# Kernel optimization log

Measured on AMD Instinct MI355X. Metric: run time of the kernel, lower is better.

## Reference

```python
import jax, jax.numpy as jnp
import numpy as np

S, B, E, H, V, L = 128, 64, 512, 1024, 10000, 2


def setup_inputs() -> dict:
    key = jax.random.key(0)
    ks = jax.random.split(key, 10)
    s = 0.02  # weight scale ~ uniform(-k,k) magnitude
    return {
        "inputs": jax.random.randint(ks[0], (S, B), 0, V),
        "hidden": jnp.zeros((L, B, H), jnp.float32),
        "emb": jax.random.normal(ks[1], (V, E), jnp.float32) * 0.1,
        "Wx0": jax.random.normal(ks[2], (3, H, E), jnp.float32) * s,
        "Uh0": jax.random.normal(ks[3], (3, H, H), jnp.float32) * s,
        "b0": jax.random.normal(ks[4], (3, H), jnp.float32) * s,
        "Wx1": jax.random.normal(ks[5], (3, H, H), jnp.float32) * s,
        "Uh1": jax.random.normal(ks[6], (3, H, H), jnp.float32) * s,
        "b1": jax.random.normal(ks[7], (3, H), jnp.float32) * s,
        "Wd": jax.random.normal(ks[8], (V, H), jnp.float32) * 0.1,
        "bd": jnp.zeros((V,), jnp.float32),
    }


def _gru_cell(xp, h, U, b):
    # xp: (3,B,H) precomputed input projections in [r,z,h] order
    r = jax.nn.sigmoid(xp[0] + h @ U[0].T + b[0])
    z = jax.nn.sigmoid(xp[1] + h @ U[1].T + b[1])
    h_tilde = jnp.tanh(xp[2] + (r * h) @ U[2].T + b[2])
    return (1.0 - z) * h + z * h_tilde


def reference(inputs, hidden, emb, Wx0, Uh0, b0, Wx1, Uh1, b1, Wd, bd):
    x_embs = emb[inputs]                                   # [S,B,E]
    # precompute layer-0 input projections across all timesteps
    xa0 = jnp.einsum("sbe,goe->sgbo", x_embs, Wx0)        # [S,3,B,H]

    def step(carry, xa0_t):
        h0, h1 = carry
        h0n = _gru_cell(xa0_t, h0, Uh0, b0)
        xp1 = jnp.einsum("bk,gok->gbo", h0n, Wx1)          # [3,B,H]
        h1n = _gru_cell(xp1, h1, Uh1, b1)
        return (h0n, h1n), h1n

    (h0f, h1f), hs1 = jax.lax.scan(step, (hidden[0], hidden[1]), xa0)
    logits = jnp.einsum("sbh,vh->sbv", hs1, Wd) + bd       # [S,B,V]
    return logits, jnp.stack([h0f, h1f])
```

## Files before the change

### kernel.cpp

```cpp
#include <hip/hip_runtime.h>
#include <hip/hip_bf16.h>

#define SLEN 128
#define BAT 64
#define EDIM 512
#define HDIM 1024
#define VOC 10000
#define VPAD 10112
#define NWG_REC 192
#define TPB_REC 512

typedef short v8s __attribute__((ext_vector_type(8)));
typedef float v4f __attribute__((ext_vector_type(4)));
typedef unsigned short u16;

__device__ __forceinline__ u16 f2bf(float f) {
  unsigned u = __float_as_uint(f);
  u += 0x7fffu + ((u >> 16) & 1u);
  return (u16)(u >> 16);
}
__device__ __forceinline__ float bf2f(u16 b) {
  return __uint_as_float(((unsigned)b) << 16);
}
__device__ __forceinline__ float sigm(float x) { return 1.f / (1.f + __expf(-x)); }
__device__ __forceinline__ float tanh_f(float x) { return 1.f - 2.f / (1.f + __expf(2.f * x)); }

__device__ __forceinline__ void st_f32(float* p, float v) {
  __hip_atomic_store(p, v, __ATOMIC_RELAXED, __HIP_MEMORY_SCOPE_AGENT);
}
__device__ __forceinline__ float ld_f32(const float* p) {
  return __hip_atomic_load(p, __ATOMIC_RELAXED, __HIP_MEMORY_SCOPE_AGENT);
}
__device__ __forceinline__ float ld_bf16(const unsigned* base, int elem) {
  unsigned pr = __hip_atomic_load(base + (elem >> 1), __ATOMIC_RELAXED, __HIP_MEMORY_SCOPE_AGENT);
  return bf2f((u16)((elem & 1) ? (pr >> 16) : (pr & 0xffffu)));
}
__device__ __forceinline__ void st_bf16_pair(unsigned* base, int elem, u16 val, int l) {
  unsigned p = (unsigned)__shfl_xor((int)val, 1);
  if ((l & 1) == 0)
    __hip_atomic_store(base + (elem >> 1), (unsigned)val | (p << 16),
                       __ATOMIC_RELAXED, __HIP_MEMORY_SCOPE_AGENT);
}

__device__ __forceinline__ void gbar(int* bar, int ph, int wg, int t) {
  asm volatile("s_waitcnt vmcnt(0) lgkmcnt(0)" ::: "memory");
  __syncthreads();
  if (t == 0)
    __hip_atomic_store(&bar[wg], ph, __ATOMIC_RELAXED, __HIP_MEMORY_SCOPE_AGENT);
  if (wg == 0) {
    if (t < 64) {
      for (;;) {
        int v0 = __hip_atomic_load(&bar[t],       __ATOMIC_RELAXED, __HIP_MEMORY_SCOPE_AGENT);
        int v1 = __hip_atomic_load(&bar[64 + t],  __ATOMIC_RELAXED, __HIP_MEMORY_SCOPE_AGENT);
        int v2 = __hip_atomic_load(&bar[128 + t], __ATOMIC_RELAXED, __HIP_MEMORY_SCOPE_AGENT);
        if (__all((v0 >= ph) & (v1 >= ph) & (v2 >= ph))) break;
        __builtin_amdgcn_s_sleep(1);
      }
      if (t == 0)
        __hip_atomic_store(&bar[256], ph, __ATOMIC_RELAXED, __HIP_MEMORY_SCOPE_AGENT);
    }
  } else if (t < 64) {
    while (__hip_atomic_load(&bar[256], __ATOMIC_RELAXED, __HIP_MEMORY_SCOPE_AGENT) < ph)
      __builtin_amdgcn_s_sleep(4);
  }
  __syncthreads();
}

__device__ __forceinline__ v4f gemm_sc(const char* apl, const char* bcl, int swz, int lk2) {
  v8s a[8];
  v4f acc0{0.f, 0.f, 0.f, 0.f}, acc1{0.f, 0.f, 0.f, 0.f};
#pragma unroll
  for (int j = 0; j < 8; ++j)
    asm volatile("global_load_dwordx4 %0, %1, off offset:%2 sc0 sc1"
                 : "=v"(a[j]) : "v"(apl), "i"(j * 64));
#pragma unroll
  for (int ks = 0; ks < 32; ++ks) {
    asm volatile("s_waitcnt vmcnt(%0)" :: "i"((ks < 24) ? 7 : (31 - ks)));
    __builtin_amdgcn_sched_barrier(0x3F6);
    v8s b = *(const v8s*)(bcl + ((ks * 64 + lk2) ^ swz));
    if (ks & 1) acc1 = __builtin_amdgcn_mfma_f32_16x16x32_bf16(a[ks & 7], b, acc1, 0, 0, 0);
    else        acc0 = __builtin_amdgcn_mfma_f32_16x16x32_bf16(a[ks & 7], b, acc0, 0, 0, 0);
    if (ks < 24)
      asm volatile("global_load_dwordx4 %0, %1, off offset:%2 sc0 sc1"
                   : "=v"(a[ks & 7]) : "v"(apl), "i"((ks + 8) * 64));
  }
  return acc0 + acc1;
}

__global__ void __launch_bounds__(512, 2) k_recur(
    const u16* __restrict__ Uh0b, const u16* __restrict__ Wx1b, const u16* __restrict__ Uh1b,
    const float* __restrict__ b0, const float* __restrict__ b1,
    const u16* __restrict__ xa0,
    float* __restrict__ h0f, u16* __restrict__ h0b,
    float* __restrict__ h1f, u16* __restrict__ h1b,
    u16* __restrict__ a2, float* __restrict__ z0,
    u16* __restrict__ a5, float* __restrict__ z1,
    u16* __restrict__ xp1,
    u16* __restrict__ hs1,
    float* __restrict__ outh,
    int* __restrict__ bar) {
  extern __shared__ char smem[];
  const int wg = blockIdx.x;
  const int t = threadIdx.x;
  const int w = t >> 6;
  const int l = t & 63;
  const int lr = l & 15;
  const int lk2 = (l >> 4) * 16;
  const int rg = w >> 1, cg = w & 1;
  const int rbase1 = rg * 16 + ((l >> 4) << 2);
  const int rbase2 = w * 16 + ((l >> 4) << 2);

  unsigned* a2u  = (unsigned*)a2;
  unsigned* a5u  = (unsigned*)a5;
  unsigned* h0bu = (unsigned*)h0b;
  unsigned* h1bu = (unsigned*)h1b;
  unsigned* xpu  = (unsigned*)xp1;

  {
    const u16* w1src; int w1row0;
    if (wg < 64)       { w1src = Uh0b; w1row0 = wg * 32; }
    else if (wg < 160) { w1src = Wx1b; w1row0 = (wg - 64) * 32; }
    else               { w1src = Uh1b; w1row0 = 2048 + (wg - 160) * 32; }
    const u16* w2src; int w2row0;
    if (wg < 64) { w2src = Uh0b; w2row0 = 2048 + wg * 16; }
    else         { w2src = Uh1b; w2row0 = (wg - 64) * 16; }
    for (int i = t; i < 4096; i += TPB_REC) {
      int c = i >> 7, j = i & 127;
      v8s v = *(const v8s*)(w1src + (size_t)(w1row0 + c) * HDIM + j * 8);
      int off = c * 2048 + ((j * 16) ^ ((c & 7) << 4));
      *(v8s*)(smem + off) = v;
    }
    for (int i = t; i < 2048; i += TPB_REC) {
      int c = i >> 7, j = i & 127;
      v8s v = *(const v8s*)(w2src + (size_t)(w2row0 + c) * HDIM + j * 8);
      int off = 65536 + c * 2048 + ((j * 16) ^ ((c & 7) << 4));
      *(v8s*)(smem + off) = v;
    }
    __syncthreads();
  }

  const char* bb1 = smem + (cg * 16 + lr) * 2048;
  const int swz1 = ((cg * 16 + lr) & 7) << 4;
  const char* bb2 = smem + 65536 + lr * 2048;
  const int swz2 = (lr & 7) << 4;

  for (int T = 0; T <= SLEN + 1; ++T) {
    if (wg < 64) {
      if (T < SLEN) {
        const int cglob = wg * 32 + cg * 16 + lr;
        const int g = cglob >> 10;
        const int o = cglob & 1023;
        const float bias = b0[g * HDIM + o];
        float xv[4], hv[4];
#pragma unroll
        for (int r = 0; r < 4; ++r) {
          int b = rbase1 + r;
          xv[r] = bf2f(xa0[((T * 3 + g) * BAT + b) * HDIM + o]);
          if (g == 0) hv[r] = ld_f32(&h0f[b * HDIM + o]);
        }
        const char* apl = (const char*)h0b + (rg * 16 + lr) * 2048 + lk2;
        v4f acc = gemm_sc(apl, bb1, swz1, lk2);
#pragma unroll
        for (int r = 0; r < 4; ++r) {
          int b = rbase1 + r;
          float s = sigm(acc[r] + xv[r] + bias);
          if (g == 0) st_bf16_pair(a2u, b * HDIM + o, f2bf(s * hv[r]), l);
          else        st_f32(&z0[b * HDIM + o], s);
        }
      }
    } else if (wg < 160) {
      if (T >= 1 && T <= SLEN) {
        const int n = (wg - 64) * 32 + cg * 16 + lr;
        const char* apl = (const char*)h0b + (rg * 16 + lr) * 2048 + lk2;
        v4f acc = gemm_sc(apl, bb1, swz1, lk2);
        unsigned* xp = xpu + (((T - 1) & 1) * (BAT * 3 * HDIM) >> 1);
#pragma unroll
        for (int r = 0; r < 4; ++r)
          st_bf16_pair(xp, (rbase1 + r) * 3072 + n, f2bf(acc[r]), l);
      }
    } else {
      if (T >= 2) {
        const int t5 = T - 2;
        const int o = (wg - 160) * 32 + cg * 16 + lr;
        const unsigned* xp = xpu + (((t5 & 1) * (BAT * 3 * HDIM)) >> 1);
        const float bias = b1[2 * HDIM + o];
        float xv[4], zv[4], hv[4];
#pragma unroll
        for (int r = 0; r < 4; ++r) {
          int b = rbase1 + r;
          xv[r] = ld_bf16(xp, b * 3072 + 2048 + o);
          zv[r] = ld_f32(&z1[b * HDIM + o]);
          hv[r] = ld_f32(&h1f[b * HDIM + o]);
        }
        const char* apl = (const char*)a5 + (rg * 16 + lr) * 2048 + lk2;
        v4f acc = gemm_sc(apl, bb1, swz1, lk2);
#pragma unroll
        for (int r = 0; r < 4; ++r) {
          int b = rbase1 + r;
          float ht = tanh_f(xv[r] + acc[r] + bias);
          float hn = (1.f - zv[r]) * hv[r] + zv[r] * ht;
          u16 hb = f2bf(hn);
          st_f32(&h1f[b * HDIM + o], hn);
          st_bf16_pair(h1bu, b * HDIM + o, hb, l);
          hs1[((size_t)t5 * BAT + b) * HDIM + o] = hb;
          if (t5 == SLEN - 1) outh[(size_t)BAT * HDIM + b * HDIM + o] = hn;
        }
      }
    }
    gbar(bar, 2 * T + 1, wg, t);
    if (w < 4) {
      if (wg < 64) {
        if (T < SLEN) {
          const int o = wg * 16 + lr;
          const float bias = b0[2 * HDIM + o];
          float xv[4], zv[4], hv[4];
#pragma unroll
          for (int r = 0; r < 4; ++r) {
            int b = rbase2 + r;
            xv[r] = bf2f(xa0[((T * 3 + 2) * BAT + b) * HDIM + o]);
            zv[r] = ld_f32(&z0[b * HDIM + o]);
            hv[r] = ld_f32(&h0f[b * HDIM + o]);
          }
          const char* apl = (const char*)a2 + (w * 16 + lr) * 2048 + lk2;
          v4f acc = gemm_sc(apl, bb2, swz2, lk2);
#pragma unroll
          for (int r = 0; r < 4; ++r) {
            int b = rbase2 + r;
            float ht = tanh_f(xv[r] + acc[r] + bias);
            float hn = (1.f - zv[r]) * hv[r] + zv[r] * ht;
            st_f32(&h0f[b * HDIM + o], hn);
            st_bf16_pair(h0bu, b * HDIM + o, f2bf(hn), l);
            if (T == SLEN - 1) outh[b * HDIM + o] = hn;
          }
        }
      } else {
        if (T >= 1 && T <= SLEN) {
          const int t4 = T - 1;
          const int cglob = (wg - 64) * 16 + lr;
          const int g = cglob >> 10;
          const int o = cglob & 1023;
          const unsigned* xp = xpu + (((t4 & 1) * (BAT * 3 * HDIM)) >> 1);
          const float bias = b1[g * HDIM + o];
          float xv[4], hv[4];
#pragma unroll
          for (int r = 0; r < 4; ++r) {
            int b = rbase2 + r;
            xv[r] = ld_bf16(xp, b * 3072 + g * HDIM + o);
            if (g == 0) hv[r] = ld_f32(&h1f[b * HDIM + o]);
          }
          const char* apl = (const char*)h1b + (w * 16 + lr) * 2048 + lk2;
          v4f acc = gemm_sc(apl, bb2, swz2, lk2);
#pragma unroll
          for (int r = 0; r < 4; ++r) {
            int b = rbase2 + r;
            float s = sigm(acc[r] + xv[r] + bias);
            if (g == 0) st_bf16_pair(a5u, b * HDIM + o, f2bf(s * hv[r]), l);
            else        st_f32(&z1[b * HDIM + o], s);
          }
        }
      }
    }
    gbar(bar, 2 * T + 2, wg, t);
  }
}

template <int MODE>
__global__ void __launch_bounds__(256) k_gemm(
    const u16* __restrict__ A, const u16* __restrict__ Bw,
    const int* __restrict__ gidx, const float* __restrict__ bias,
    void* __restrict__ Out) {
  constexpr int K = MODE ? 1024 : 512;
  constexpr int NB_N = MODE ? (VPAD / 128) : (3072 / 128);

  __shared__ u16 sA[128 * 64];
  __shared__ u16 sB[128 * 64];

  const int nwg = gridDim.x;
  const int cpx = nwg >> 3;
  const int bid = blockIdx.x;
  const int swz = (bid & 7) * cpx + (bid >> 3);
  const int bm = swz / NB_N, bn = swz % NB_N;
  const int m0 = bm * 128, n0 = bn * 128;

  const int t = threadIdx.x;
  const int w = t >> 6, l = t & 63;
  const int lr = l & 15, lk = (l >> 4) * 8;
  const int wm = (w >> 1) * 64, wn = (w & 1) * 64;
  const int kc = (t & 7) * 8;

  int arowg[4];
#pragma unroll
  for (int i = 0; i < 4; ++i) {
    int row = m0 + i * 32 + (t >> 3);
    arowg[i] = (MODE == 0) ? gidx[row] : row;
  }
  int brow[4];
#pragma unroll
  for (int i = 0; i < 4; ++i) brow[i] = n0 + i * 32 + (t >> 3);

  v4f acc[4][4];
#pragma unroll
  for (int mi = 0; mi < 4; ++mi)
#pragma unroll
    for (int ni = 0; ni < 4; ++ni) acc[mi][ni] = v4f{0.f, 0.f, 0.f, 0.f};

  for (int k0 = 0; k0 < K; k0 += 64) {
    __syncthreads();
#pragma unroll
    for (int i = 0; i < 4; ++i) {
      const u16* src = A + (size_t)arowg[i] * K + k0 + kc;
      __builtin_amdgcn_global_load_lds((const __attribute__((address_space(1))) void*)src,
                                       (__attribute__((address_space(3))) void*)(sA + i * 2048 + w * 512),
                                       16, 0, 0);
    }
#pragma unroll
    for (int i = 0; i < 4; ++i) {
      const u16* src = Bw + (size_t)brow[i] * K + k0 + kc;
      __builtin_amdgcn_global_load_lds((const __attribute__((address_space(1))) void*)src,
                                       (__attribute__((address_space(3))) void*)(sB + i * 2048 + w * 512),
                                       16, 0, 0);
    }
    asm volatile("s_waitcnt vmcnt(0)" ::: "memory");
    __syncthreads();
#pragma unroll
    for (int ks = 0; ks < 2; ++ks) {
      v8s af[4], bfr[4];
#pragma unroll
      for (int mi = 0; mi < 4; ++mi) af[mi] = *(const v8s*)&sA[(wm + mi * 16 + lr) * 64 + ks * 32 + lk];
#pragma unroll
      for (int ni = 0; ni < 4; ++ni) bfr[ni] = *(const v8s*)&sB[(wn + ni * 16 + lr) * 64 + ks * 32 + lk];
#pragma unroll
      for (int mi = 0; mi < 4; ++mi)
#pragma unroll
        for (int ni = 0; ni < 4; ++ni)
          acc[mi][ni] = __builtin_amdgcn_mfma_f32_16x16x32_bf16(af[mi], bfr[ni], acc[mi][ni], 0, 0, 0);
    }
  }

#pragma unroll
  for (int mi = 0; mi < 4; ++mi)
#pragma unroll
    for (int ni = 0; ni < 4; ++ni)
#pragma unroll
      for (int r = 0; r < 4; ++r) {
        int grow = m0 + wm + mi * 16 + ((l >> 4) << 2) + r;
        int gcol = n0 + wn + ni * 16 + lr;
        float v = acc[mi][ni][r];
        if (MODE == 0) {
          int s = grow >> 6, b = grow & 63;
          int g = gcol >> 10, o = gcol & 1023;
          ((u16*)Out)[(((size_t)s * 3 + g) * BAT + b) * HDIM + o] = f2bf(v);
        } else {
          if (gcol < VOC) ((float*)Out)[(size_t)grow * VOC + gcol] = v + bias[gcol];
        }
      }
}

__global__ void k_cvt(const float* __restrict__ src, u16* __restrict__ dst, int n, int nsrc) {
  int i = (blockIdx.x * 256 + threadIdx.x) * 4;
  if (i >= n) return;
#pragma unroll
  for (int j = 0; j < 4; ++j) {
    int idx = i + j;
    if (idx < n) dst[idx] = (idx < nsrc) ? f2bf(src[idx]) : (u16)0;
  }
}

__global__ void k_init(const float* __restrict__ hidden,
                       float* h0f, u16* h0b, float* h1f, u16* h1b, int* bar) {
  int i = blockIdx.x * 256 + threadIdx.x;
  if (i < BAT * HDIM) {
    float v0 = hidden[i];
    float v1 = hidden[BAT * HDIM + i];
    h0f[i] = v0; h0b[i] = f2bf(v0);
    h1f[i] = v1; h1b[i] = f2bf(v1);
  }
  if (i < 512) bar[i] = 0;
}

extern "C" void kernel_launch(void* const* d_in, const int* in_sizes, int n_in,
                              void* d_out, int out_size, void* d_ws, size_t ws_size,
                              hipStream_t stream) {
  const int*   inp = (const int*)d_in[0];
  const float* hid = (const float*)d_in[1];
  const float* emb = (const float*)d_in[2];
  const float* Wx0 = (const float*)d_in[3];
  const float* Uh0 = (const float*)d_in[4];
  const float* b0  = (const float*)d_in[5];
  const float* Wx1 = (const float*)d_in[6];
  const float* Uh1 = (const float*)d_in[7];
  const float* b1  = (const float*)d_in[8];
  const float* Wd  = (const float*)d_in[9];
  const float* bd  = (const float*)d_in[10];

  char* ws = (char*)d_ws;
  size_t off = 0;
  auto alloc = [&](size_t bytes) {
    void* p = ws + off;
    off = (off + bytes + 255) & ~(size_t)255;
    return p;
  };
  u16* emb_b = (u16*)alloc(sizeof(u16) * (size_t)VOC * EDIM);
  u16* Wx0_b = (u16*)alloc(sizeof(u16) * 3 * HDIM * EDIM);
  u16* Uh0_b = (u16*)alloc(sizeof(u16) * 3 * HDIM * HDIM);
  u16* Wx1_b = (u16*)alloc(sizeof(u16) * 3 * HDIM * HDIM);
  u16* Uh1_b = (u16*)alloc(sizeof(u16) * 3 * HDIM * HDIM);
  u16* Wd_b  = (u16*)alloc(sizeof(u16) * (size_t)VPAD * HDIM);
  u16* xa0_b = (u16*)alloc(sizeof(u16) * (size_t)SLEN * 3 * BAT * HDIM);
  u16* hs1_b = (u16*)alloc(sizeof(u16) * (size_t)SLEN * BAT * HDIM);
  u16* xp1   = (u16*)alloc(sizeof(u16) * 2 * BAT * 3 * HDIM);
  float* h0f = (float*)alloc(sizeof(float) * BAT * HDIM);
  float* h1f = (float*)alloc(sizeof(float) * BAT * HDIM);
  u16* h0b   = (u16*)alloc(sizeof(u16) * BAT * HDIM);
  u16* h1b   = (u16*)alloc(sizeof(u16) * BAT * HDIM);
  u16* a2    = (u16*)alloc(sizeof(u16) * BAT * HDIM);
  u16* a5    = (u16*)alloc(sizeof(u16) * BAT * HDIM);
  float* z0  = (float*)alloc(sizeof(float) * BAT * HDIM);
  float* z1  = (float*)alloc(sizeof(float) * BAT * HDIM);
  int* bar   = (int*)alloc(sizeof(int) * 512);

  float* logits = (float*)d_out;
  float* outh = logits + (size_t)SLEN * BAT * VOC;

  auto cvt = [&](const float* s, u16* d, int n, int nsrc) {
    k_cvt<<<dim3((n / 4 + 255) / 256), dim3(256), 0, stream>>>(s, d, n, nsrc);
  };
  cvt(emb, emb_b, VOC * EDIM, VOC * EDIM);
  cvt(Wx0, Wx0_b, 3 * HDIM * EDIM, 3 * HDIM * EDIM);
  cvt(Uh0, Uh0_b, 3 * HDIM * HDIM, 3 * HDIM * HDIM);
  cvt(Wx1, Wx1_b, 3 * HDIM * HDIM, 3 * HDIM * HDIM);
  cvt(Uh1, Uh1_b, 3 * HDIM * HDIM, 3 * HDIM * HDIM);
  cvt(Wd, Wd_b, VPAD * HDIM, VOC * HDIM);
  k_init<<<dim3(256), dim3(256), 0, stream>>>(hid, h0f, h0b, h1f, h1b, bar);

  k_gemm<0><<<dim3(64 * 24), dim3(256), 0, stream>>>(emb_b, Wx0_b, inp, (const float*)nullptr, (void*)xa0_b);

  (void)hipFuncSetAttribute(reinterpret_cast<const void*>(k_recur),
                            hipFuncAttributeMaxDynamicSharedMemorySize, 96 * 1024);
  k_recur<<<dim3(NWG_REC), dim3(TPB_REC), 96 * 1024, stream>>>(
      Uh0_b, Wx1_b, Uh1_b, b0, b1, xa0_b,
      h0f, h0b, h1f, h1b, a2, z0, a5, z1, xp1, hs1_b, outh, bar);

  k_gemm<1><<<dim3(64 * 79), dim3(256), 0, stream>>>(hs1_b, Wd_b, (const int*)nullptr, bd, d_out);
}
```

Before: 3.015 ms.

## Stage activation tiles through LDS and rebalance second-phase GEMM across fewer workgroups

Replaces per-wave direct global loads of the activation operand with a cooperative, double-buffered LDS staging pipeline, so each 64x1024 activation tile is fetched once per workgroup instead of once per wave row-group. The second barrier phase now uses 96 workgroups each computing 32 columns with all 8 waves, instead of 192 workgroups using only 4 waves. The grid barrier becomes decentralized, with every workgroup polling all flags rather than waiting on a master's release flag. LDS grows to 144KB, which limits occupancy to one workgroup per CU and adds per-chunk __syncthreads inside the GEMM.

```diff
diff --git a/kernel.cpp b/kernel.cpp
--- a/kernel.cpp
+++ b/kernel.cpp
@@ -47,47 +47,58 @@
   __syncthreads();
   if (t == 0)
     __hip_atomic_store(&bar[wg], ph, __ATOMIC_RELAXED, __HIP_MEMORY_SCOPE_AGENT);
-  if (wg == 0) {
-    if (t < 64) {
-      for (;;) {
-        int v0 = __hip_atomic_load(&bar[t],       __ATOMIC_RELAXED, __HIP_MEMORY_SCOPE_AGENT);
-        int v1 = __hip_atomic_load(&bar[64 + t],  __ATOMIC_RELAXED, __HIP_MEMORY_SCOPE_AGENT);
-        int v2 = __hip_atomic_load(&bar[128 + t], __ATOMIC_RELAXED, __HIP_MEMORY_SCOPE_AGENT);
-        if (__all((v0 >= ph) & (v1 >= ph) & (v2 >= ph))) break;
-        __builtin_amdgcn_s_sleep(1);
-      }
-      if (t == 0)
-        __hip_atomic_store(&bar[256], ph, __ATOMIC_RELAXED, __HIP_MEMORY_SCOPE_AGENT);
-    }
-  } else if (t < 64) {
-    while (__hip_atomic_load(&bar[256], __ATOMIC_RELAXED, __HIP_MEMORY_SCOPE_AGENT) < ph)
-      __builtin_amdgcn_s_sleep(4);
+  if (t < 64) {
+    for (;;) {
+      int v0 = __hip_atomic_load(&bar[t],       __ATOMIC_RELAXED, __HIP_MEMORY_SCOPE_AGENT);
+      int v1 = __hip_atomic_load(&bar[64 + t],  __ATOMIC_RELAXED, __HIP_MEMORY_SCOPE_AGENT);
+      int v2 = __hip_atomic_load(&bar[128 + t], __ATOMIC_RELAXED, __HIP_MEMORY_SCOPE_AGENT);
+      if (__all((v0 >= ph) & (v1 >= ph) & (v2 >= ph))) break;
+      __builtin_amdgcn_s_sleep(1);
+    }
   }
   __syncthreads();
 }
 
-__device__ __forceinline__ v4f gemm_sc(const char* apl, const char* bcl, int swz, int lk2) {
-  v8s a[8];
-  v4f acc0{0.f, 0.f, 0.f, 0.f}, acc1{0.f, 0.f, 0.f, 0.f};
-#pragma unroll
-  for (int j = 0; j < 8; ++j)
-    asm volatile("global_load_dwordx4 %0, %1, off offset:%2 sc0 sc1"
-                 : "=v"(a[j]) : "v"(apl), "i"(j * 64));
-#pragma unroll
-  for (int ks = 0; ks < 32; ++ks) {
-    asm volatile("s_waitcnt vmcnt(%0)" :: "i"((ks < 24) ? 7 : (31 - ks)));
-    __builtin_amdgcn_sched_barrier(0x3F6);
-    v8s b = *(const v8s*)(bcl + ((ks * 64 + lk2) ^ swz));
-    if (ks & 1) acc1 = __builtin_amdgcn_mfma_f32_16x16x32_bf16(a[ks & 7], b, acc1, 0, 0, 0);
-    else        acc0 = __builtin_amdgcn_mfma_f32_16x16x32_bf16(a[ks & 7], b, acc0, 0, 0, 0);
-    if (ks < 24)
+__device__ __forceinline__ v4f gemm_staged(const char* Asrc, char* stage,
+                                           const char* bb, int swz,
+                                           int t, int rg, int lr, int lk2) {
+  const char* gp = Asrc + (t >> 3) * 2048 + (t & 7) * 16;
+  char* wp = stage + (t >> 3) * 128 + ((((t & 7) * 16)) ^ (((t >> 3) & 7) << 4));
+  const char* rp = stage + (rg * 16 + lr) * 128;
+  v4f acc{0.f, 0.f, 0.f, 0.f};
+  v8s sreg[3];
+  asm volatile("global_load_dwordx4 %0, %1, off sc0 sc1" : "=v"(sreg[0]) : "v"(gp));
+  asm volatile("global_load_dwordx4 %0, %1, off offset:128 sc0 sc1" : "=v"(sreg[1]) : "v"(gp));
+  asm volatile("global_load_dwordx4 %0, %1, off offset:256 sc0 sc1" : "=v"(sreg[2]) : "v"(gp));
+  asm volatile("s_waitcnt vmcnt(2)" ::: "memory");
+  __builtin_amdgcn_sched_barrier(0);
+  *(v8s*)wp = sreg[0];
+  __syncthreads();
+#pragma unroll
+  for (int c = 0; c < 16; ++c) {
+    if (c < 13)
       asm volatile("global_load_dwordx4 %0, %1, off offset:%2 sc0 sc1"
-                   : "=v"(a[ks & 7]) : "v"(apl), "i"((ks + 8) * 64));
-  }
-  return acc0 + acc1;
-}
-
-__global__ void __launch_bounds__(512, 2) k_recur(
+                   : "=v"(sreg[c % 3]) : "v"(gp), "i"((c + 3) * 128));
+    if (c < 15) {
+      if (c < 13)       asm volatile("s_waitcnt vmcnt(2)" ::: "memory");
+      else if (c == 13) asm volatile("s_waitcnt vmcnt(1)" ::: "memory");
+      else              asm volatile("s_waitcnt vmcnt(0)" ::: "memory");
+      __builtin_amdgcn_sched_barrier(0);
+      *(v8s*)(wp + ((c + 1) & 1) * 8192) = sreg[(c + 1) % 3];
+    }
+    const char* buf = rp + (c & 1) * 8192;
+#pragma unroll
+    for (int ls = 0; ls < 2; ++ls) {
+      v8s a = *(const v8s*)(buf + ((ls * 64 + lk2) ^ swz));
+      v8s b = *(const v8s*)(bb + (((c * 2 + ls) * 64 + lk2) ^ swz));
+      acc = __builtin_amdgcn_mfma_f32_16x16x32_bf16(a, b, acc, 0, 0, 0);
+    }
+    __syncthreads();
+  }
+  return acc;
+}
+
+__global__ void __launch_bounds__(TPB_REC, 2) k_recur(
     const u16* __restrict__ Uh0b, const u16* __restrict__ Wx1b, const u16* __restrict__ Uh1b,
     const float* __restrict__ b0, const float* __restrict__ b1,
     const u16* __restrict__ xa0,
@@ -107,8 +118,9 @@
   const int lr = l & 15;
   const int lk2 = (l >> 4) * 16;
   const int rg = w >> 1, cg = w & 1;
-  const int rbase1 = rg * 16 + ((l >> 4) << 2);
-  const int rbase2 = w * 16 + ((l >> 4) << 2);
+  const int rbase = rg * 16 + ((l >> 4) << 2);
+  const int swz = (lr & 7) << 4;
+  char* stage = smem + 131072;
 
   unsigned* a2u  = (unsigned*)a2;
   unsigned* a5u  = (unsigned*)a5;
@@ -121,28 +133,26 @@
     if (wg < 64)       { w1src = Uh0b; w1row0 = wg * 32; }
     else if (wg < 160) { w1src = Wx1b; w1row0 = (wg - 64) * 32; }
     else               { w1src = Uh1b; w1row0 = 2048 + (wg - 160) * 32; }
-    const u16* w2src; int w2row0;
-    if (wg < 64) { w2src = Uh0b; w2row0 = 2048 + wg * 16; }
-    else         { w2src = Uh1b; w2row0 = (wg - 64) * 16; }
     for (int i = t; i < 4096; i += TPB_REC) {
       int c = i >> 7, j = i & 127;
       v8s v = *(const v8s*)(w1src + (size_t)(w1row0 + c) * HDIM + j * 8);
-      int off = c * 2048 + ((j * 16) ^ ((c & 7) << 4));
-      *(v8s*)(smem + off) = v;
-    }
-    for (int i = t; i < 2048; i += TPB_REC) {
-      int c = i >> 7, j = i & 127;
-      v8s v = *(const v8s*)(w2src + (size_t)(w2row0 + c) * HDIM + j * 8);
-      int off = 65536 + c * 2048 + ((j * 16) ^ ((c & 7) << 4));
-      *(v8s*)(smem + off) = v;
+      *(v8s*)(smem + c * 2048 + ((j * 16) ^ ((c & 7) << 4))) = v;
+    }
+    if (wg < 96) {
+      const u16* w2src; int w2row0;
+      if (wg < 32) { w2src = Uh0b; w2row0 = 2048 + wg * 32; }
+      else         { w2src = Uh1b; w2row0 = (wg - 32) * 32; }
+      for (int i = t; i < 4096; i += TPB_REC) {
+        int c = i >> 7, j = i & 127;
+        v8s v = *(const v8s*)(w2src + (size_t)(w2row0 + c) * HDIM + j * 8);
+        *(v8s*)(smem + 65536 + c * 2048 + ((j * 16) ^ ((c & 7) << 4))) = v;
+      }
     }
     __syncthreads();
   }
 
   const char* bb1 = smem + (cg * 16 + lr) * 2048;
-  const int swz1 = ((cg * 16 + lr) & 7) << 4;
-  const char* bb2 = smem + 65536 + lr * 2048;
-  const int swz2 = (lr & 7) << 4;
+  const char* bb2 = smem + 65536 + (cg * 16 + lr) * 2048;
 
   for (int T = 0; T <= SLEN + 1; ++T) {
     if (wg < 64) {
@@ -154,15 +164,14 @@
         float xv[4], hv[4];
 #pragma unroll
         for (int r = 0; r < 4; ++r) {
-          int b = rbase1 + r;
+          int b = rbase + r;
           xv[r] = bf2f(xa0[((T * 3 + g) * BAT + b) * HDIM + o]);
           if (g == 0) hv[r] = ld_f32(&h0f[b * HDIM + o]);
         }
-        const char* apl = (const char*)h0b + (rg * 16 + lr) * 2048 + lk2;
-        v4f acc = gemm_sc(apl, bb1, swz1, lk2);
-#pragma unroll
-        for (int r = 0; r < 4; ++r) {
-          int b = rbase1 + r;
+        v4f acc = gemm_staged((const char*)h0b, stage, bb1, swz, t, rg, lr, lk2);
+#pragma unroll
+        for (int r = 0; r < 4; ++r) {
+          int b = rbase + r;
           float s = sigm(acc[r] + xv[r] + bias);
           if (g == 0) st_bf16_pair(a2u, b * HDIM + o, f2bf(s * hv[r]), l);
           else        st_f32(&z0[b * HDIM + o], s);
@@ -171,12 +180,11 @@
     } else if (wg < 160) {
       if (T >= 1 && T <= SLEN) {
         const int n = (wg - 64) * 32 + cg * 16 + lr;
-        const char* apl = (const char*)h0b + (rg * 16 + lr) * 2048 + lk2;
-        v4f acc = gemm_sc(apl, bb1, swz1, lk2);
-        unsigned* xp = xpu + (((T - 1) & 1) * (BAT * 3 * HDIM) >> 1);
+        v4f acc = gemm_staged((const char*)h0b, stage, bb1, swz, t, rg, lr, lk2);
+        unsigned* xp = xpu + ((((T - 1) & 1) * (BAT * 3 * HDIM)) >> 1);
 #pragma unroll
         for (int r = 0; r < 4; ++r)
-          st_bf16_pair(xp, (rbase1 + r) * 3072 + n, f2bf(acc[r]), l);
+          st_bf16_pair(xp, (rbase + r) * 3072 + n, f2bf(acc[r]), l);
       }
     } else {
       if (T >= 2) {
@@ -184,20 +192,19 @@
         const int o = (wg - 160) * 32 + cg * 16 + lr;
         const unsigned* xp = xpu + (((t5 & 1) * (BAT * 3 * HDIM)) >> 1);
         const float bias = b1[2 * HDIM + o];
-        float xv[4], zv[4], hv[4];
-#pragma unroll
-        for (int r = 0; r < 4; ++r) {
-          int b = rbase1 + r;
-          xv[r] = ld_bf16(xp, b * 3072 + 2048 + o);
+        float pv[4], zv[4], hv[4];
+#pragma unroll
+        for (int r = 0; r < 4; ++r) {
+          int b = rbase + r;
+          pv[r] = ld_bf16(xp, b * 3072 + 2048 + o);
           zv[r] = ld_f32(&z1[b * HDIM + o]);
           hv[r] = ld_f32(&h1f[b * HDIM + o]);
         }
-        const char* apl = (const char*)a5 + (rg * 16 + lr) * 2048 + lk2;
-        v4f acc = gemm_sc(apl, bb1, swz1, lk2);
-#pragma unroll
-        for (int r = 0; r < 4; ++r) {
-          int b = rbase1 + r;
-          float ht = tanh_f(xv[r] + acc[r] + bias);
+        v4f acc = gemm_staged((const char*)a5, stage, bb1, swz, t, rg, lr, lk2);
+#pragma unroll
+        for (int r = 0; r < 4; ++r) {
+          int b = rbase + r;
+          float ht = tanh_f(pv[r] + acc[r] + bias);
           float hn = (1.f - zv[r]) * hv[r] + zv[r] * ht;
           u16 hb = f2bf(hn);
           st_f32(&h1f[b * HDIM + o], hn);
@@ -208,55 +215,51 @@
       }
     }
     gbar(bar, 2 * T + 1, wg, t);
-    if (w < 4) {
-      if (wg < 64) {
-        if (T < SLEN) {
-          const int o = wg * 16 + lr;
-          const float bias = b0[2 * HDIM + o];
-          float xv[4], zv[4], hv[4];
-#pragma unroll
-          for (int r = 0; r < 4; ++r) {
-            int b = rbase2 + r;
-            xv[r] = bf2f(xa0[((T * 3 + 2) * BAT + b) * HDIM + o]);
-            zv[r] = ld_f32(&z0[b * HDIM + o]);
-            hv[r] = ld_f32(&h0f[b * HDIM + o]);
-          }
-          const char* apl = (const char*)a2 + (w * 16 + lr) * 2048 + lk2;
-          v4f acc = gemm_sc(apl, bb2, swz2, lk2);
-#pragma unroll
-          for (int r = 0; r < 4; ++r) {
-            int b = rbase2 + r;
-            float ht = tanh_f(xv[r] + acc[r] + bias);
-            float hn = (1.f - zv[r]) * hv[r] + zv[r] * ht;
-            st_f32(&h0f[b * HDIM + o], hn);
-            st_bf16_pair(h0bu, b * HDIM + o, f2bf(hn), l);
-            if (T == SLEN - 1) outh[b * HDIM + o] = hn;
-          }
-        }
-      } else {
-        if (T >= 1 && T <= SLEN) {
-          const int t4 = T - 1;
-          const int cglob = (wg - 64) * 16 + lr;
-          const int g = cglob >> 10;
-          const int o = cglob & 1023;
-          const unsigned* xp = xpu + (((t4 & 1) * (BAT * 3 * HDIM)) >> 1);
-          const float bias = b1[g * HDIM + o];
-          float xv[4], hv[4];
-#pragma unroll
-          for (int r = 0; r < 4; ++r) {
-            int b = rbase2 + r;
-            xv[r] = ld_bf16(xp, b * 3072 + g * HDIM + o);
-            if (g == 0) hv[r] = ld_f32(&h1f[b * HDIM + o]);
-          }
-          const char* apl = (const char*)h1b + (w * 16 + lr) * 2048 + lk2;
-          v4f acc = gemm_sc(apl, bb2, swz2, lk2);
-#pragma unroll
-          for (int r = 0; r < 4; ++r) {
-            int b = rbase2 + r;
-            float s = sigm(acc[r] + xv[r] + bias);
-            if (g == 0) st_bf16_pair(a5u, b * HDIM + o, f2bf(s * hv[r]), l);
-            else        st_f32(&z1[b * HDIM + o], s);
-          }
+    if (wg < 32) {
+      if (T < SLEN) {
+        const int o = wg * 32 + cg * 16 + lr;
+        const float bias = b0[2 * HDIM + o];
+        float xv[4], zv[4], hv[4];
+#pragma unroll
+        for (int r = 0; r < 4; ++r) {
+          int b = rbase + r;
+          xv[r] = bf2f(xa0[((T * 3 + 2) * BAT + b) * HDIM + o]);
+          zv[r] = ld_f32(&z0[b * HDIM + o]);
+          hv[r] = ld_f32(&h0f[b * HDIM + o]);
+        }
+        v4f acc = gemm_staged((const char*)a2, stage, bb2, swz, t, rg, lr, lk2);
+#pragma unroll
+        for (int r = 0; r < 4; ++r) {
+          int b = rbase + r;
+          float ht = tanh_f(xv[r] + acc[r] + bias);
+          float hn = (1.f - zv[r]) * hv[r] + zv[r] * ht;
+          st_f32(&h0f[b * HDIM + o], hn);
+          st_bf16_pair(h0bu, b * HDIM + o, f2bf(hn), l);
+          if (T == SLEN - 1) outh[b * HDIM + o] = hn;
+        }
+      }
+    } else if (wg < 96) {
+      if (T >= 1 && T <= SLEN) {
+        const int t4 = T - 1;
+        const int cglob = (wg - 32) * 32 + cg * 16 + lr;
+        const int g = cglob >> 10;
+        const int o = cglob & 1023;
+        const unsigned* xp = xpu + (((t4 & 1) * (BAT * 3 * HDIM)) >> 1);
+        const float bias = b1[g * HDIM + o];
+        float pv[4], hv[4];
+#pragma unroll
+        for (int r = 0; r < 4; ++r) {
+          int b = rbase + r;
+          pv[r] = ld_bf16(xp, b * 3072 + g * HDIM + o);
+          if (g == 0) hv[r] = ld_f32(&h1f[b * HDIM + o]);
+        }
+        v4f acc = gemm_staged((const char*)h1b, stage, bb2, swz, t, rg, lr, lk2);
+#pragma unroll
+        for (int r = 0; r < 4; ++r) {
+          int b = rbase + r;
+          float s = sigm(acc[r] + pv[r] + bias);
+          if (g == 0) st_bf16_pair(a5u, b * HDIM + o, f2bf(s * hv[r]), l);
+          else        st_f32(&z1[b * HDIM + o], s);
         }
       }
     }
@@ -436,8 +439,8 @@
   k_gemm<0><<<dim3(64 * 24), dim3(256), 0, stream>>>(emb_b, Wx0_b, inp, (const float*)nullptr, (void*)xa0_b);
 
   (void)hipFuncSetAttribute(reinterpret_cast<const void*>(k_recur),
-                            hipFuncAttributeMaxDynamicSharedMemorySize, 96 * 1024);
-  k_recur<<<dim3(NWG_REC), dim3(TPB_REC), 96 * 1024, stream>>>(
+                            hipFuncAttributeMaxDynamicSharedMemorySize, 147456);
+  k_recur<<<dim3(NWG_REC), dim3(TPB_REC), 147456, stream>>>(
       Uh0_b, Wx1_b, Uh1_b, b0, b1, xa0_b,
       h0f, h0b, h1f, h1b, a2, z0, a5, z1, xp1, hs1_b, outh, bar);
 
```

Result: faster. 2.730 ms (-9.5%).
